# Kernel optimization log

Hardware: AMD Instinct MI355X
Metric: run time of the kernel (lower is better)

Reference implementation:

```python
import jax, jax.numpy as jnp
import numpy as np

B, N, P, D = 16, 358, 72, 96
ND, H, K = 64, 4, 10
HL = H // 2
HG = H - HL
NH = 4  # temporal attention heads


def ln(x, g, b, eps=1e-5):
    m = x.mean(-1, keepdims=True)
    v = ((x - m) ** 2).mean(-1, keepdims=True)
    return (x - m) / jnp.sqrt(v + eps) * g + b


def topk_sparsify(adj, k):
    # row-wise top-k masking + renormalization, vectorized over all leading dims
    shp = adj.shape
    n = shp[-1]
    flat = adj.reshape(-1, shp[-2], n)
    M, R = flat.shape[0], flat.shape[1]
    _, idx = jax.lax.top_k(flat, k)  # (M,R,k)
    mask = jnp.zeros(flat.shape, flat.dtype).at[
        jnp.arange(M)[:, None, None], jnp.arange(R)[None, :, None], idx].set(1.0)
    sp = flat * mask
    sp = sp / (sp.sum(-1, keepdims=True) + 1e-8)
    return sp.reshape(shp)


def forward(patch_features, local_e1, local_e2, global_e1, global_e2, static_e2,
            temperature, pos_enc, wq, bq, wk, bk, wv, bv, wo, bo, tn_g, tn_b,
            de_w1, de_b1, de_g1, de_beta1, de_w2, de_b2, de_g2, de_beta2,
            gnn_w, gnn_b, gnn_g, gnn_beta, gf_w, gf_b,
            ee_w1, ee_b1, ee_g, ee_beta, ee_w2, ee_b2, ee_w3, ee_b3):
    # ---- static multi-head graphs (batched over heads instead of python loop) ----
    adj_l = jax.nn.relu(jnp.einsum('hnd,hdm->hnm', local_e1, local_e2))
    t_l = jnp.clip(temperature[:HL] * 2.0, 0.1, 5.0)
    adj_l = jax.nn.softmax(adj_l / t_l[:, None, None], axis=-1)
    adj_g = jax.nn.relu(jnp.einsum('hnd,hdm->hnm', global_e1, global_e2))
    t_g = jnp.clip(temperature[HL:] * 0.5, 0.1, 2.0)
    adj_g = jax.nn.softmax(adj_g / t_g[:, None, None], axis=-1)
    static_adjs = jnp.concatenate([adj_l, adj_g], axis=0)  # (H,N,N)

    # ---- dynamic graphs ----
    b, n, p, d = patch_features.shape
    pr = patch_features.reshape(b * n, p, d)
    x = pr + pos_enc[:, :p]
    hd = d // NH
    q = (x @ wq + bq).reshape(-1, p, NH, hd).transpose(0, 2, 1, 3)
    kk = (x @ wk + bk).reshape(-1, p, NH, hd).transpose(0, 2, 1, 3)
    v = (x @ wv + bv).reshape(-1, p, NH, hd).transpose(0, 2, 1, 3)
    att = jax.nn.softmax(jnp.einsum('bhqd,bhkd->bhqk', q, kk) / np.float32(np.sqrt(hd)), axis=-1)
    o = jnp.einsum('bhqk,bhkd->bhqd', att, v).transpose(0, 2, 1, 3).reshape(-1, p, d)
    attended = o @ wo + bo  # (BN,P,D)
    imp = jax.nn.softmax(attended.mean(-1), axis=1)  # (BN,P)
    node = (attended * imp[..., None]).sum(1) + pr.mean(1)
    node = ln(node, tn_g, tn_b).reshape(b, n, d)
    h1 = jax.nn.gelu(ln(node @ de_w1 + de_b1, de_g1, de_beta1), approximate=False)
    dyn = ln(h1 @ de_w2 + de_b2, de_g2, de_beta2)  # (B,N,ND)
    for i in range(2):  # 2 structurally distinct GNN layers, batched over B
        sim = jax.nn.softmax(jnp.einsum('bnd,bmd->bnm', dyn, dyn) / 0.2, axis=-1)
        agg = jnp.einsum('bnm,bmd->bnd', sim, dyn)
        out = jax.nn.gelu(ln(agg @ gnn_w[i] + gnn_b[i], gnn_g[i], gnn_beta[i]), approximate=False)
        dyn = out + dyn
    dsim = jax.nn.relu(jnp.einsum('bnd,hdm->bhnm', dyn, static_e2))
    t_d = jnp.clip(temperature, 0.1, 2.0)
    dynamic_adjs = jax.nn.softmax(dsim / t_d[None, :, None, None], axis=-1)  # (B,H,N,N)

    static_adjs = topk_sparsify(static_adjs, K)
    dynamic_adjs = topk_sparsify(dynamic_adjs, K)

    # ---- static/dynamic fusion ----
    node_f = patch_features.mean(2)  # (B,N,D)
    fw = jax.nn.sigmoid(node_f @ gf_w + gf_b)  # (B,N,H)
    w = jnp.transpose(fw, (0, 2, 1))[..., None]  # (B,H,N,1), broadcast over columns
    fused = (1.0 - w) * static_adjs[None] + w * dynamic_adjs  # (B,H,N,N)

    # ---- edge encoder over head dim ----
    mh = jnp.transpose(fused, (0, 2, 3, 1))  # (B,N,N,H)
    e = jax.nn.gelu(ln(mh @ ee_w1 + ee_b1, ee_g, ee_beta), approximate=False)
    e = jax.nn.gelu(e @ ee_w2 + ee_b2, approximate=False)
    e = (e @ ee_w3 + ee_b3)[..., 0]  # (B,N,N)
    final = jax.nn.sigmoid(e) * fused.mean(1)
    return final, static_adjs, dynamic_adjs


def setup_inputs() -> dict:
    key = jax.random.key(0)
    ks = jax.random.split(key, 20)
    r = lambda i, shape, s=0.05: jax.random.normal(ks[i], shape, dtype=jnp.float32) * s
    z = lambda shape: jnp.zeros(shape, jnp.float32)
    o = lambda shape: jnp.ones(shape, jnp.float32)
    return dict(
        patch_features=r(0, (B, N, P, D), 1.0),
        local_e1=r(1, (HL, N, ND // 2), 0.1),
        local_e2=r(2, (HL, ND // 2, N), 0.1),
        global_e1=r(3, (HG, N, ND), 0.1),
        global_e2=r(4, (HG, ND, N), 0.1),
        static_e2=r(5, (H, ND, N), 0.1),
        temperature=jnp.full((H,), 0.5, jnp.float32),
        pos_enc=r(6, (1, 72, D), 0.02),
        wq=r(7, (D, D)), bq=z((D,)),
        wk=r(8, (D, D)), bk=z((D,)),
        wv=r(9, (D, D)), bv=z((D,)),
        wo=r(10, (D, D)), bo=z((D,)),
        tn_g=o((D,)), tn_b=z((D,)),
        de_w1=r(11, (D, 2 * ND)), de_b1=z((2 * ND,)),
        de_g1=o((2 * ND,)), de_beta1=z((2 * ND,)),
        de_w2=r(12, (2 * ND, ND)), de_b2=z((ND,)),
        de_g2=o((ND,)), de_beta2=z((ND,)),
        gnn_w=r(13, (2, ND, ND)), gnn_b=z((2, ND)),
        gnn_g=o((2, ND)), gnn_beta=z((2, ND)),
        gf_w=r(14, (D, H)), gf_b=z((H,)),
        ee_w1=r(15, (H, 4 * H)), ee_b1=z((4 * H,)),
        ee_g=o((4 * H,)), ee_beta=z((4 * H,)),
        ee_w2=r(16, (4 * H, 2 * H)), ee_b2=z((2 * H,)),
        ee_w3=r(17, (2 * H, 1)), ee_b3=z((1,)),
    )


def reference(patch_features, local_e1, local_e2, global_e1, global_e2, static_e2,
              temperature, pos_enc, wq, bq, wk, bk, wv, bv, wo, bo, tn_g, tn_b,
              de_w1, de_b1, de_g1, de_beta1, de_w2, de_b2, de_g2, de_beta2,
              gnn_w, gnn_b, gnn_g, gnn_beta, gf_w, gf_b,
              ee_w1, ee_b1, ee_g, ee_beta, ee_w2, ee_b2, ee_w3, ee_b3):
    return forward(patch_features, local_e1, local_e2, global_e1, global_e2, static_e2,
                   temperature, pos_enc, wq, bq, wk, bk, wv, bv, wo, bo, tn_g, tn_b,
                   de_w1, de_b1, de_g1, de_beta1, de_w2, de_b2, de_g2, de_beta2,
                   gnn_w, gnn_b, gnn_g, gnn_beta, gf_w, gf_b,
                   ee_w1, ee_b1, ee_g, ee_beta, ee_w2, ee_b2, ee_w3, ee_b3)
```

## Files before the change

kernel.cpp:

```cpp
#include <hip/hip_runtime.h>
#include <hip/hip_bf16.h>

#define B_ 16
#define N_ 358
#define P_ 72
#define D_ 96
#define ND_ 64
#define H_ 4
#define NH_ 4
#define HD_ 24
#define K_ 10
#define BN_ (B_*N_)
#define NN_ (N_*N_)
#define RPW_ 6
#define NR5 5

__device__ __forceinline__ float gelu_f(float x){ return 0.5f*x*(1.0f+erff(x*0.7071067811865476f)); }
__device__ __forceinline__ float sigm_f(float x){ return 1.0f/(1.0f+expf(-x)); }

__global__ __launch_bounds__(512, 2) void attn_kernel(
    const float* __restrict__ patch, const float* __restrict__ pos,
    const float* __restrict__ wq, const float* __restrict__ bq,
    const float* __restrict__ wk, const float* __restrict__ bk,
    const float* __restrict__ wv, const float* __restrict__ bv,
    const float* __restrict__ wo, const float* __restrict__ bo,
    const float* __restrict__ tng, const float* __restrict__ tnb,
    float* __restrict__ node_out, float* __restrict__ meanpr_out)
{
    __shared__ __align__(16) float pool[14904];
    __shared__ float rr[80];
    __shared__ float nb[D_];
    __shared__ float st2[2];

    float* const xs   = pool;
    float* const qh   = pool;
    float* const khT  = pool + 2240;
    float* const vhT  = pool + 4568;
    float* const att  = pool + 6584;
    float* const obuf = pool + 12664;
    float* const ats  = pool;

    const int tid = threadIdx.x;
    const int tc  = tid & 31;
    const int tr  = tid >> 5;
    const int rbase = tr * NR5;
    const int bn  = blockIdx.x;
    const float* pr = patch + (size_t)bn * (P_*D_);

    float mpr = 0.f;
    if (tid < D_) {
        #pragma unroll 1
        for (int p = 0; p < P_; ++p) mpr += pr[p*D_+tid];
        mpr *= (1.0f/P_);
        meanpr_out[(size_t)bn*D_ + tid] = mpr;
    }

    #pragma unroll 1
    for (int e = tid; e < 80*100; e += 512) {
        const int row = e / 100, col = e - row*100;
        xs[e] = (row < P_ && col < D_) ? (pr[row*D_+col] + pos[row*D_+col]) : 0.f;
    }
    __syncthreads();

    float aq[3][NR5], ak[3][NR5], av[3][NR5];

#define P1_LOOP(WP, BP, ACC)                                                 \
    {                                                                        \
        _Pragma("unroll")                                                    \
        for (int j = 0; j < 3; ++j) {                                        \
            const float vb = BP[tc + 32*j];                                  \
            _Pragma("unroll")                                                \
            for (int i = 0; i < NR5; ++i) ACC[j][i] = vb;                    \
        }                                                                    \
        _Pragma("unroll 1")                                                  \
        for (int k0 = 0; k0 < D_; k0 += 4) {                                 \
            float4 xv[NR5];                                                  \
            _Pragma("unroll")                                                \
            for (int i = 0; i < NR5; ++i)                                    \
                xv[i] = *reinterpret_cast<const float4*>(&xs[(rbase+i)*100 + k0]); \
            float w4[3][4];                                                  \
            _Pragma("unroll")                                                \
            for (int j = 0; j < 3; ++j) {                                    \
                const int c = tc + 32*j;                                     \
                _Pragma("unroll")                                            \
                for (int kk = 0; kk < 4; ++kk)                               \
                    w4[j][kk] = WP[(k0+kk)*D_ + c];                          \
            }                                                                \
            _Pragma("unroll")                                                \
            for (int j = 0; j < 3; ++j)                                      \
                _Pragma("unroll")                                            \
                for (int i = 0; i < NR5; ++i)                                \
                    ACC[j][i] += xv[i].x*w4[j][0] + xv[i].y*w4[j][1]         \
                               + xv[i].z*w4[j][2] + xv[i].w*w4[j][3];        \
        }                                                                    \
    }

    P1_LOOP(wq, bq, aq)
    P1_LOOP(wk, bk, ak)
    P1_LOOP(wv, bv, av)
#undef P1_LOOP

    __syncthreads();

    const float rs = 0.20412414523193154f;

    float ao[3][NR5];
    #pragma unroll
    for (int j = 0; j < 3; ++j) {
        const float vbo = bo[tc + 32*j];
        #pragma unroll
        for (int i = 0; i < NR5; ++i) ao[j][i] = vbo;
    }

    auto stage = [&](int hh) {
        #pragma unroll
        for (int j = 0; j < 3; ++j) {
            const int c = tc + 32*j;
            const int dl = c - HD_*hh;
            if ((unsigned)dl < (unsigned)HD_) {
                #pragma unroll
                for (int i = 0; i < NR5; ++i) {
                    const int row = rbase + i;
                    qh [row*28 + dl] = aq[j][i] * rs;
                    khT[dl*97 + row] = ak[j][i];
                    vhT[dl*84 + row] = av[j][i];
                }
            }
        }
    };

    stage(0);
    __syncthreads();

    #pragma unroll 1
    for (int h = 0; h < NH_; ++h) {
        float sc[3][NR5];
        #pragma unroll
        for (int j = 0; j < 3; ++j)
            #pragma unroll
            for (int i = 0; i < NR5; ++i) sc[j][i] = 0.f;
        #pragma unroll 1
        for (int d0 = 0; d0 < HD_; d0 += 2) {
            float2 qv[NR5];
            #pragma unroll
            for (int i = 0; i < NR5; ++i)
                qv[i] = *reinterpret_cast<const float2*>(&qh[(rbase+i)*28 + d0]);
            float kv[3][2];
            #pragma unroll
            for (int j = 0; j < 3; ++j) {
                const int jn = tc + 32*j;
                kv[j][0] = khT[(d0+0)*97 + jn];
                kv[j][1] = khT[(d0+1)*97 + jn];
            }
            #pragma unroll
            for (int j = 0; j < 3; ++j)
                #pragma unroll
                for (int i = 0; i < NR5; ++i)
                    sc[j][i] += qv[i].x*kv[j][0] + qv[i].y*kv[j][1];
        }

        #pragma unroll
        for (int i = 0; i < NR5; ++i) {
            float m = fmaxf(sc[0][i], sc[1][i]);
            if (tc < 8) m = fmaxf(m, sc[2][i]);
            #pragma unroll
            for (int s = 1; s < 32; s <<= 1) m = fmaxf(m, __shfl_xor(m, s, 32));
            const float e0 = expf(sc[0][i]-m);
            const float e1 = expf(sc[1][i]-m);
            const float e2 = (tc < 8) ? expf(sc[2][i]-m) : 0.f;
            float sm = e0 + e1 + e2;
            #pragma unroll
            for (int s = 1; s < 32; s <<= 1) sm += __shfl_xor(sm, s, 32);
            const float inv = 1.0f/sm;
            const int row = rbase + i;
            att[row*76 + tc]      = e0*inv;
            att[row*76 + tc + 32] = e1*inv;
            if (tc < 8) att[row*76 + tc + 64] = e2*inv;
        }
        __syncthreads();

        if (tc < HD_) {
            float ov[NR5];
            #pragma unroll
            for (int i = 0; i < NR5; ++i) ov[i] = 0.f;
            #pragma unroll 1
            for (int j0 = 0; j0 < P_; j0 += 4) {
                const float4 vv = *reinterpret_cast<const float4*>(&vhT[tc*84 + j0]);
                #pragma unroll
                for (int i = 0; i < NR5; ++i) {
                    const float4 pa = *reinterpret_cast<const float4*>(&att[(rbase+i)*76 + j0]);
                    ov[i] += pa.x*vv.x + pa.y*vv.y + pa.z*vv.z + pa.w*vv.w;
                }
            }
            #pragma unroll
            for (int i = 0; i < NR5; ++i) obuf[(rbase+i)*28 + tc] = ov[i];
        }
        __syncthreads();

        #pragma unroll 1
        for (int d0 = 0; d0 < HD_; d0 += 2) {
            float2 ov2[NR5];
            #pragma unroll
            for (int i = 0; i < NR5; ++i)
                ov2[i] = *reinterpret_cast<const float2*>(&obuf[(rbase+i)*28 + d0]);
            float w2[3][2];
            #pragma unroll
            for (int j = 0; j < 3; ++j) {
                const int c = tc + 32*j;
                w2[j][0] = wo[(HD_*h + d0 + 0)*D_ + c];
                w2[j][1] = wo[(HD_*h + d0 + 1)*D_ + c];
            }
            #pragma unroll
            for (int j = 0; j < 3; ++j)
                #pragma unroll
                for (int i = 0; i < NR5; ++i)
                    ao[j][i] += ov2[i].x*w2[j][0] + ov2[i].y*w2[j][1];
        }
        if (h < NH_-1) stage(h+1);
        __syncthreads();
    }

    #pragma unroll
    for (int j = 0; j < 3; ++j) {
        const int c = tc + 32*j;
        #pragma unroll
        for (int i = 0; i < NR5; ++i) ats[(rbase+i)*100 + c] = ao[j][i];
    }
    __syncthreads();

    if (tid < P_) {
        const float* ar = ats + tid*100;
        float s = 0.f;
        #pragma unroll 1
        for (int d = 0; d < D_; ++d) s += ar[d];
        rr[tid] = s*(1.0f/D_);
    }
    __syncthreads();
    if (tid < 64) {
        const float a0 = rr[tid];
        const float a1 = (tid < 8) ? rr[64+tid] : -3.0e38f;
        float mx = fmaxf(a0, a1);
        #pragma unroll
        for (int s = 1; s < 64; s <<= 1) mx = fmaxf(mx, __shfl_xor(mx, s));
        const float e0 = expf(a0-mx);
        const float e1 = (tid < 8) ? expf(a1-mx) : 0.f;
        float sm = e0 + e1;
        #pragma unroll
        for (int s = 1; s < 64; s <<= 1) sm += __shfl_xor(sm, s);
        const float inv = 1.0f/sm;
        rr[tid] = e0*inv;
        if (tid < 8) rr[64+tid] = e1*inv;
    }
    __syncthreads();
    if (tid < D_) {
        float s = 0.f;
        #pragma unroll 1
        for (int i = 0; i < P_; ++i) s += ats[i*100+tid]*rr[i];
        nb[tid] = s + mpr;
    }
    __syncthreads();
    if (tid < 64) {
        const float x0 = nb[tid];
        const float x1 = (tid < 32) ? nb[64+tid] : 0.f;
        float sm = x0 + x1;
        float sq = x0*x0 + x1*x1;
        #pragma unroll
        for (int s = 1; s < 64; s <<= 1) { sm += __shfl_xor(sm, s); sq += __shfl_xor(sq, s); }
        if (tid == 0) {
            const float m = sm*(1.0f/D_);
            const float v = sq*(1.0f/D_) - m*m;
            st2[0] = m; st2[1] = rsqrtf(v + 1e-5f);
        }
    }
    __syncthreads();
    if (tid < D_) {
        const float y = (nb[tid]-st2[0])*st2[1]*tng[tid] + tnb[tid];
        node_out[(size_t)bn*D_+tid] = y;
    }
}

__global__ __launch_bounds__(128) void enc1_kernel(
    const float* __restrict__ node, const float* __restrict__ w1, const float* __restrict__ b1,
    const float* __restrict__ g1, const float* __restrict__ be1, float* __restrict__ h1)
{
    __shared__ float nr[D_];
    __shared__ float buf[128];
    __shared__ float st2[2];
    const int tid = threadIdx.x; const int bn = blockIdx.x;
    if (tid < D_) nr[tid] = node[(size_t)bn*D_+tid];
    __syncthreads();
    float s = b1[tid];
    for (int c = 0; c < D_; ++c) s += nr[c]*w1[c*128+tid];
    buf[tid] = s;
    __syncthreads();
    if (tid == 0) {
        float m=0.f; for(int d=0;d<128;++d) m+=buf[d]; m *= (1.0f/128.0f);
        float v=0.f; for(int d=0;d<128;++d){ float df=buf[d]-m; v+=df*df; } v *= (1.0f/128.0f);
        st2[0]=m; st2[1]=rsqrtf(v+1e-5f);
    }
    __syncthreads();
    float y = (buf[tid]-st2[0])*st2[1]*g1[tid] + be1[tid];
    h1[(size_t)bn*128+tid] = gelu_f(y);
}

__global__ __launch_bounds__(64) void enc2_kernel(
    const float* __restrict__ h1, const float* __restrict__ w2, const float* __restrict__ b2,
    const float* __restrict__ g2, const float* __restrict__ be2, float* __restrict__ dyn)
{
    __shared__ float hr[128];
    __shared__ float buf[ND_];
    __shared__ float st2[2];
    const int tid = threadIdx.x; const int bn = blockIdx.x;
    hr[tid] = h1[(size_t)bn*128+tid];
    hr[tid+64] = h1[(size_t)bn*128+64+tid];
    __syncthreads();
    float s = b2[tid];
    for (int c = 0; c < 128; ++c) s += hr[c]*w2[c*ND_+tid];
    buf[tid] = s;
    __syncthreads();
    if (tid == 0) {
        float m=0.f; for(int d=0;d<ND_;++d) m+=buf[d]; m *= (1.0f/ND_);
        float v=0.f; for(int d=0;d<ND_;++d){ float df=buf[d]-m; v+=df*df; } v *= (1.0f/ND_);
        st2[0]=m; st2[1]=rsqrtf(v+1e-5f);
    }
    __syncthreads();
    dyn[(size_t)bn*ND_+tid] = (buf[tid]-st2[0])*st2[1]*g2[tid] + be2[tid];
}

__global__ __launch_bounds__(256) void gnn_kernel(
    const float* __restrict__ din, float* __restrict__ dout,
    const float* __restrict__ gw, const float* __restrict__ gb,
    const float* __restrict__ gg, const float* __restrict__ gbe, int layer)
{
    __shared__ float dq[ND_];
    __shared__ float prob[N_];
    __shared__ float red[256];
    __shared__ float aggp[4*ND_];
    __shared__ float buf[ND_];
    __shared__ float st2[2];
    const int tid = threadIdx.x; const int bn = blockIdx.x;
    const int b = bn / N_;
    const float* base = din + (size_t)b*N_*ND_;
    if (tid < ND_) dq[tid] = din[(size_t)bn*ND_+tid];
    __syncthreads();

    float lmax = -1e30f;
    for (int m = tid; m < N_; m += 256) {
        const float* rm = base + (size_t)m*ND_;
        float s = 0.f;
        for (int c = 0; c < ND_; ++c) s += dq[c]*rm[c];
        s *= 5.0f;
        prob[m] = s;
        lmax = fmaxf(lmax, s);
    }
    red[tid]=lmax; __syncthreads();
    for (int st=128; st>0; st>>=1){ if(tid<st) red[tid]=fmaxf(red[tid],red[tid+st]); __syncthreads(); }
    const float mx = red[0]; __syncthreads();
    float lsum = 0.f;
    for (int m=tid; m<N_; m+=256){ float ev=expf(prob[m]-mx); prob[m]=ev; lsum+=ev; }
    red[tid]=lsum; __syncthreads();
    for (int st=128; st>0; st>>=1){ if(tid<st) red[tid]+=red[tid+st]; __syncthreads(); }
    const float inv = 1.0f/red[0]; __syncthreads();
    for (int m=tid; m<N_; m+=256) prob[m]*=inv;
    __syncthreads();

    {
        const int part = tid >> 6, d = tid & 63;
        float s = 0.f;
        for (int m = part; m < N_; m += 4) s += prob[m]*base[(size_t)m*ND_+d];
        aggp[part*ND_+d] = s;
    }
    __syncthreads();
    if (tid < ND_)
        aggp[tid] = aggp[tid]+aggp[ND_+tid]+aggp[2*ND_+tid]+aggp[3*ND_+tid];
    __syncthreads();
    if (tid < ND_) {
        float t = gb[layer*ND_+tid];
        for (int c = 0; c < ND_; ++c) t += aggp[c]*gw[(layer*ND_+c)*ND_+tid];
        buf[tid] = t;
    }
    __syncthreads();
    if (tid == 0) {
        float m=0.f; for(int d=0;d<ND_;++d) m+=buf[d]; m *= (1.0f/ND_);
        float v=0.f; for(int d=0;d<ND_;++d){ float df=buf[d]-m; v+=df*df; } v *= (1.0f/ND_);
        st2[0]=m; st2[1]=rsqrtf(v+1e-5f);
    }
    __syncthreads();
    if (tid < ND_) {
        float y = (buf[tid]-st2[0])*st2[1]*gg[layer*ND_+tid] + gbe[layer*ND_+tid];
        dout[(size_t)bn*ND_+tid] = gelu_f(y) + dq[tid];
    }
}

__device__ __forceinline__ void wave_softmax_topk_store(
    float lv[RPW_], int lane, float* __restrict__ outrow)
{
    float mx = 0.f;
    #pragma unroll
    for (int j=0;j<RPW_;++j) mx = fmaxf(mx, lv[j]);
    #pragma unroll
    for (int s=1;s<64;s<<=1) mx = fmaxf(mx, __shfl_xor(mx, s));
    float sm = 0.f;
    #pragma unroll
    for (int j=0;j<RPW_;++j) {
        const int m = lane + 64*j;
        const float e = (m < N_) ? expf(lv[j]-mx) : 0.f;
        lv[j] = e; sm += e;
    }
    #pragma unroll
    for (int s=1;s<64;s<<=1) sm += __shfl_xor(sm, s);
    const float inv = 1.0f/sm;
    #pragma unroll
    for (int j=0;j<RPW_;++j) lv[j] *= inv;

    unsigned sel = 0u;
    float ksum = 0.f;
    for (int it = 0; it < K_; ++it) {
        float bv = -1.f; int bm = 0x7fffffff;
        #pragma unroll
        for (int j=0;j<RPW_;++j) {
            const int m = lane + 64*j;
            if (m < N_ && !((sel>>j)&1u) && lv[j] > bv) { bv = lv[j]; bm = m; }
        }
        #pragma unroll
        for (int s=1;s<64;s<<=1) {
            const float ov = __shfl_xor(bv, s);
            const int   om = __shfl_xor(bm, s);
            if (ov > bv || (ov == bv && om < bm)) { bv = ov; bm = om; }
        }
        ksum += bv;
        if ((bm & 63) == lane) sel |= 1u << (bm >> 6);
    }
    const float dn = 1.0f/(ksum + 1e-8f);
    #pragma unroll
    for (int j=0;j<RPW_;++j) {
        const int m = lane + 64*j;
        if (m < N_) outrow[m] = ((sel>>j)&1u) ? lv[j]*dn : 0.f;
    }
}

__global__ __launch_bounds__(256) void static_adj_kernel(
    const float* __restrict__ le1, const float* __restrict__ le2,
    const float* __restrict__ ge1, const float* __restrict__ ge2,
    const float* __restrict__ temp, float* __restrict__ outs)
{
    __shared__ float e1l[4][ND_];
    const int tid = threadIdx.x;
    const int wv = tid >> 6, lane = tid & 63;
    const int r = blockIdx.x*4 + wv;
    const int h = r / N_, n = r % N_;
    if (h < 2) { if (lane < 32) e1l[wv][lane] = le1[(h*N_+n)*32+lane]; }
    else       { e1l[wv][lane] = ge1[((h-2)*N_+n)*64+lane]; }
    __syncthreads();
    const float t = temp[h];
    const float tl = (h < 2) ? fminf(fmaxf(t*2.0f,0.1f),5.0f) : fminf(fmaxf(t*0.5f,0.1f),2.0f);
    const float invt = 1.0f/tl;
    float lv[RPW_];
    #pragma unroll
    for (int j=0;j<RPW_;++j) lv[j] = 0.f;
    if (h < 2) {
        for (int c = 0; c < 32; ++c) {
            const float dc = e1l[wv][c];
            const float* sr = le2 + (size_t)(h*32+c)*N_;
            #pragma unroll
            for (int j=0;j<RPW_;++j) {
                const int m = lane + 64*j;
                if (m < N_) lv[j] += dc*sr[m];
            }
        }
    } else {
        for (int c = 0; c < 64; ++c) {
            const float dc = e1l[wv][c];
            const float* sr = ge2 + (size_t)((h-2)*64+c)*N_;
            #pragma unroll
            for (int j=0;j<RPW_;++j) {
                const int m = lane + 64*j;
                if (m < N_) lv[j] += dc*sr[m];
            }
        }
    }
    #pragma unroll
    for (int j=0;j<RPW_;++j) lv[j] = fmaxf(lv[j],0.f)*invt;
    wave_softmax_topk_store(lv, lane, outs + (size_t)r*N_);
}

__global__ __launch_bounds__(256) void dyn_adj_kernel(
    const float* __restrict__ dyn, const float* __restrict__ se2,
    const float* __restrict__ temp, float* __restrict__ outd)
{
    __shared__ float dql[4][ND_];
    const int tid = threadIdx.x;
    const int wv = tid >> 6, lane = tid & 63;
    const int r = blockIdx.x*4 + wv;
    const int b = r / (H_*N_);
    const int rem = r % (H_*N_);
    const int h = rem / N_, n = rem % N_;
    dql[wv][lane] = dyn[((size_t)(b*N_+n))*ND_ + lane];
    __syncthreads();
    const float invt = 1.0f/fminf(fmaxf(temp[h],0.1f),2.0f);
    float lv[RPW_];
    #pragma unroll
    for (int j=0;j<RPW_;++j) lv[j] = 0.f;
    const float* sb = se2 + (size_t)h*ND_*N_;
    for (int c = 0; c < ND_; ++c) {
        const float dc = dql[wv][c];
        const float* sr = sb + (size_t)c*N_;
        #pragma unroll
        for (int j=0;j<RPW_;++j) {
            const int m = lane + 64*j;
            if (m < N_) lv[j] += dc*sr[m];
        }
    }
    #pragma unroll
    for (int j=0;j<RPW_;++j) lv[j] = fmaxf(lv[j],0.f)*invt;
    wave_softmax_topk_store(lv, lane, outd + ((size_t)(b*H_+h)*N_+n)*(size_t)N_);
}

__global__ __launch_bounds__(256) void fw_kernel(
    const float* __restrict__ meanpr, const float* __restrict__ gfw,
    const float* __restrict__ gfb, float* __restrict__ wf)
{
    const int gid = blockIdx.x*256 + threadIdx.x;
    if (gid >= BN_*H_) return;
    const int bn = gid >> 2, h = gid & 3;
    float s = gfb[h];
    const float* mp = meanpr + (size_t)bn*D_;
    for (int c=0;c<D_;++c) s += mp[c]*gfw[c*H_+h];
    wf[gid] = sigm_f(s);
}

__global__ __launch_bounds__(256) void edge_kernel(
    const float* __restrict__ staticf, const float* __restrict__ dynf,
    const float* __restrict__ wf,
    const float* __restrict__ ew1, const float* __restrict__ eb1,
    const float* __restrict__ eg,  const float* __restrict__ ebe,
    const float* __restrict__ ew2, const float* __restrict__ eb2,
    const float* __restrict__ ew3, const float* __restrict__ eb3,
    float* __restrict__ outf)
{
    __shared__ float w1s[64], w2s[128], b1s[16], gs[16], bes[16], b2s[8], w3s[8];
    __shared__ float b3v;
    const int tid = threadIdx.x;
    if (tid < 64)                 w1s[tid]     = ew1[tid];
    else if (tid < 192)           w2s[tid-64]  = ew2[tid-64];
    else if (tid < 208)           b1s[tid-192] = eb1[tid-192];
    else if (tid < 224)           gs[tid-208]  = eg[tid-208];
    else if (tid < 240)           bes[tid-224] = ebe[tid-224];
    else if (tid < 248)           b2s[tid-240] = eb2[tid-240];
    else                          w3s[tid-248] = ew3[tid-248];
    if (tid == 0) b3v = eb3[0];
    __syncthreads();

    const size_t gid = (size_t)blockIdx.x*256 + tid;
    if (gid >= (size_t)B_*NN_) return;
    const int m = (int)(gid % N_);
    const size_t t1 = gid / N_;
    const int n = (int)(t1 % N_);
    const int b = (int)(t1 / N_);

    const float* wrow = wf + ((size_t)(b*N_+n))*4;
    float mh[4]; float msum = 0.f;
    #pragma unroll
    for (int h=0; h<4; ++h) {
        float w  = wrow[h];
        float st = staticf[((size_t)(h*N_+n))*N_ + m];
        float da = dynf[(((size_t)(b*4+h))*N_+n)*(size_t)N_ + m];
        float f = (1.0f-w)*st + w*da;
        mh[h] = f; msum += f;
    }
    float e16[16]; float mean = 0.f;
    #pragma unroll
    for (int j=0;j<16;++j) {
        float s = b1s[j];
        #pragma unroll
        for (int h=0;h<4;++h) s += mh[h]*w1s[h*16+j];
        e16[j] = s; mean += s;
    }
    mean *= (1.0f/16.0f);
    float var = 0.f;
    #pragma unroll
    for (int j=0;j<16;++j){ float df=e16[j]-mean; var += df*df; }
    var *= (1.0f/16.0f);
    const float rinv = rsqrtf(var + 1e-5f);
    #pragma unroll
    for (int j=0;j<16;++j) e16[j] = gelu_f((e16[j]-mean)*rinv*gs[j] + bes[j]);
    float e8[8];
    #pragma unroll
    for (int o=0;o<8;++o) {
        float s = b2s[o];
        #pragma unroll
        for (int j=0;j<16;++j) s += e16[j]*w2s[j*8+o];
        e8[o] = gelu_f(s);
    }
    float e = b3v;
    #pragma unroll
    for (int o=0;o<8;++o) e += e8[o]*w3s[o];
    outf[gid] = sigm_f(e) * (msum*0.25f);
}

extern "C" void kernel_launch(void* const* d_in, const int* in_sizes, int n_in,
                              void* d_out, int out_size, void* d_ws, size_t ws_size,
                              hipStream_t stream)
{
    const float* patch = (const float*)d_in[0];
    const float* le1   = (const float*)d_in[1];
    const float* le2   = (const float*)d_in[2];
    const float* ge1   = (const float*)d_in[3];
    const float* ge2   = (const float*)d_in[4];
    const float* se2   = (const float*)d_in[5];
    const float* temp  = (const float*)d_in[6];
    const float* pos   = (const float*)d_in[7];
    const float* wq    = (const float*)d_in[8];
    const float* bq    = (const float*)d_in[9];
    const float* wk    = (const float*)d_in[10];
    const float* bk    = (const float*)d_in[11];
    const float* wv    = (const float*)d_in[12];
    const float* bv    = (const float*)d_in[13];
    const float* wo    = (const float*)d_in[14];
    const float* bo    = (const float*)d_in[15];
    const float* tng   = (const float*)d_in[16];
    const float* tnb   = (const float*)d_in[17];
    const float* dw1   = (const float*)d_in[18];
    const float* db1   = (const float*)d_in[19];
    const float* dg1   = (const float*)d_in[20];
    const float* dbe1  = (const float*)d_in[21];
    const float* dw2   = (const float*)d_in[22];
    const float* db2   = (const float*)d_in[23];
    const float* dg2   = (const float*)d_in[24];
    const float* dbe2  = (const float*)d_in[25];
    const float* gw    = (const float*)d_in[26];
    const float* gb    = (const float*)d_in[27];
    const float* gg    = (const float*)d_in[28];
    const float* gbe   = (const float*)d_in[29];
    const float* gfw   = (const float*)d_in[30];
    const float* gfb   = (const float*)d_in[31];
    const float* ew1   = (const float*)d_in[32];
    const float* eb1   = (const float*)d_in[33];
    const float* eg    = (const float*)d_in[34];
    const float* ebe   = (const float*)d_in[35];
    const float* ew2   = (const float*)d_in[36];
    const float* eb2   = (const float*)d_in[37];
    const float* ew3   = (const float*)d_in[38];
    const float* eb3   = (const float*)d_in[39];
    (void)in_sizes; (void)n_in; (void)out_size; (void)ws_size;

    float* ws      = (float*)d_ws;
    float* meanpr  = ws;
    float* node    = meanpr + (size_t)BN_*D_;
    float* h1      = node   + (size_t)BN_*D_;
    float* dyn0    = h1     + (size_t)BN_*128;
    float* dyn1    = node;
    float* wfuse   = h1;

    float* out        = (float*)d_out;
    float* out_final  = out;
    float* out_static = out + (size_t)B_*NN_;
    float* out_dyn    = out_static + (size_t)H_*NN_;

    attn_kernel<<<BN_, 512, 0, stream>>>(patch,pos,wq,bq,wk,bk,wv,bv,wo,bo,tng,tnb,node,meanpr);
    enc1_kernel<<<BN_, 128, 0, stream>>>(node,dw1,db1,dg1,dbe1,h1);
    enc2_kernel<<<BN_, 64,  0, stream>>>(h1,dw2,db2,dg2,dbe2,dyn0);
    gnn_kernel<<<BN_, 256, 0, stream>>>(dyn0,dyn1,gw,gb,gg,gbe,0);
    gnn_kernel<<<BN_, 256, 0, stream>>>(dyn1,dyn0,gw,gb,gg,gbe,1);
    static_adj_kernel<<<H_*N_/4, 256, 0, stream>>>(le1,le2,ge1,ge2,temp,out_static);
    dyn_adj_kernel<<<B_*H_*N_/4, 256, 0, stream>>>(dyn0,se2,temp,out_dyn);
    fw_kernel<<<(BN_*H_+255)/256, 256, 0, stream>>>(meanpr,gfw,gfb,wfuse);
    edge_kernel<<<((size_t)B_*NN_+255)/256, 256, 0, stream>>>(
        out_static,out_dyn,wfuse,ew1,eb1,eg,ebe,ew2,eb2,ew3,eb3,out_final);
}
```

Measured before the change: 2.969 ms.

## Pre-transpose attention weights and vectorize QKV, score and output projections

Adds a small kernel that transposes wq/wk/wv/wo into workspace so the attention kernel can read weights as float4 along the reduction dimension instead of scalar strided loads. K is now stored row-major with a 28-float stride, so score dot products read float4 from both Q and K. Softmax exponentials switch to fast __expf. This trades an extra launch, more shared memory and possible LDS bank conflicts for fewer load instructions, with slightly lower exp precision.

```diff
diff --git a/kernel.cpp b/kernel.cpp
--- a/kernel.cpp
+++ b/kernel.cpp
@@ -18,26 +18,42 @@
 __device__ __forceinline__ float gelu_f(float x){ return 0.5f*x*(1.0f+erff(x*0.7071067811865476f)); }
 __device__ __forceinline__ float sigm_f(float x){ return 1.0f/(1.0f+expf(-x)); }
 
+__global__ __launch_bounds__(256) void transw_kernel(
+    const float* __restrict__ wq, const float* __restrict__ wk,
+    const float* __restrict__ wv, const float* __restrict__ wo,
+    float* __restrict__ wqT, float* __restrict__ wkT,
+    float* __restrict__ wvT, float* __restrict__ woT)
+{
+    const int gid = blockIdx.x*256 + threadIdx.x;
+    if (gid >= 4*D_*D_) return;
+    const int mat = gid / (D_*D_);
+    const int idx = gid - mat*(D_*D_);
+    const int c = idx / D_, k = idx - c*D_;
+    const float* src = (mat==0)?wq:(mat==1)?wk:(mat==2)?wv:wo;
+    float* dst = (mat==0)?wqT:(mat==1)?wkT:(mat==2)?wvT:woT;
+    dst[idx] = src[k*D_ + c];
+}
+
 __global__ __launch_bounds__(512, 2) void attn_kernel(
     const float* __restrict__ patch, const float* __restrict__ pos,
-    const float* __restrict__ wq, const float* __restrict__ bq,
-    const float* __restrict__ wk, const float* __restrict__ bk,
-    const float* __restrict__ wv, const float* __restrict__ bv,
-    const float* __restrict__ wo, const float* __restrict__ bo,
+    const float* __restrict__ wqT, const float* __restrict__ bq,
+    const float* __restrict__ wkT, const float* __restrict__ bk,
+    const float* __restrict__ wvT, const float* __restrict__ bv,
+    const float* __restrict__ woT, const float* __restrict__ bo,
     const float* __restrict__ tng, const float* __restrict__ tnb,
     float* __restrict__ node_out, float* __restrict__ meanpr_out)
 {
-    __shared__ __align__(16) float pool[14904];
+    __shared__ __align__(16) float pool[15264];
     __shared__ float rr[80];
     __shared__ float nb[D_];
     __shared__ float st2[2];
 
     float* const xs   = pool;
     float* const qh   = pool;
-    float* const khT  = pool + 2240;
-    float* const vhT  = pool + 4568;
-    float* const att  = pool + 6584;
-    float* const obuf = pool + 12664;
+    float* const kh   = pool + 2240;
+    float* const vhT  = pool + 4928;
+    float* const att  = pool + 6944;
+    float* const obuf = pool + 13024;
     float* const ats  = pool;
 
     const int tid = threadIdx.x;
@@ -64,7 +80,7 @@
 
     float aq[3][NR5], ak[3][NR5], av[3][NR5];
 
-#define P1_LOOP(WP, BP, ACC)                                                 \
+#define P1_LOOP(WTP, BP, ACC)                                                \
     {                                                                        \
         _Pragma("unroll")                                                    \
         for (int j = 0; j < 3; ++j) {                                        \
@@ -78,26 +94,22 @@
             _Pragma("unroll")                                                \
             for (int i = 0; i < NR5; ++i)                                    \
                 xv[i] = *reinterpret_cast<const float4*>(&xs[(rbase+i)*100 + k0]); \
-            float w4[3][4];                                                  \
+            float4 w4[3];                                                    \
             _Pragma("unroll")                                                \
-            for (int j = 0; j < 3; ++j) {                                    \
-                const int c = tc + 32*j;                                     \
-                _Pragma("unroll")                                            \
-                for (int kk = 0; kk < 4; ++kk)                               \
-                    w4[j][kk] = WP[(k0+kk)*D_ + c];                          \
-            }                                                                \
+            for (int j = 0; j < 3; ++j)                                      \
+                w4[j] = *reinterpret_cast<const float4*>(&WTP[(tc+32*j)*D_ + k0]); \
             _Pragma("unroll")                                                \
             for (int j = 0; j < 3; ++j)                                      \
                 _Pragma("unroll")                                            \
                 for (int i = 0; i < NR5; ++i)                                \
-                    ACC[j][i] += xv[i].x*w4[j][0] + xv[i].y*w4[j][1]         \
-                               + xv[i].z*w4[j][2] + xv[i].w*w4[j][3];        \
+                    ACC[j][i] += xv[i].x*w4[j].x + xv[i].y*w4[j].y           \
+                               + xv[i].z*w4[j].z + xv[i].w*w4[j].w;          \
         }                                                                    \
     }
 
-    P1_LOOP(wq, bq, aq)
-    P1_LOOP(wk, bk, ak)
-    P1_LOOP(wv, bv, av)
+    P1_LOOP(wqT, bq, aq)
+    P1_LOOP(wkT, bk, ak)
+    P1_LOOP(wvT, bv, av)
 #undef P1_LOOP
 
     __syncthreads();
@@ -122,7 +134,7 @@
                 for (int i = 0; i < NR5; ++i) {
                     const int row = rbase + i;
                     qh [row*28 + dl] = aq[j][i] * rs;
-                    khT[dl*97 + row] = ak[j][i];
+                    kh [row*28 + dl] = ak[j][i];
                     vhT[dl*84 + row] = av[j][i];
                 }
             }
@@ -140,23 +152,23 @@
             #pragma unroll
             for (int i = 0; i < NR5; ++i) sc[j][i] = 0.f;
         #pragma unroll 1
-        for (int d0 = 0; d0 < HD_; d0 += 2) {
-            float2 qv[NR5];
+        for (int d0 = 0; d0 < HD_; d0 += 4) {
+            float4 qv[NR5];
             #pragma unroll
             for (int i = 0; i < NR5; ++i)
-                qv[i] = *reinterpret_cast<const float2*>(&qh[(rbase+i)*28 + d0]);
-            float kv[3][2];
+                qv[i] = *reinterpret_cast<const float4*>(&qh[(rbase+i)*28 + d0]);
+            float4 kv[3];
             #pragma unroll
             for (int j = 0; j < 3; ++j) {
                 const int jn = tc + 32*j;
-                kv[j][0] = khT[(d0+0)*97 + jn];
-                kv[j][1] = khT[(d0+1)*97 + jn];
+                kv[j] = *reinterpret_cast<const float4*>(&kh[jn*28 + d0]);
             }
             #pragma unroll
             for (int j = 0; j < 3; ++j)
                 #pragma unroll
                 for (int i = 0; i < NR5; ++i)
-                    sc[j][i] += qv[i].x*kv[j][0] + qv[i].y*kv[j][1];
+                    sc[j][i] += qv[i].x*kv[j].x + qv[i].y*kv[j].y
+                              + qv[i].z*kv[j].z + qv[i].w*kv[j].w;
         }
 
         #pragma unroll
@@ -165,9 +177,9 @@
             if (tc < 8) m = fmaxf(m, sc[2][i]);
             #pragma unroll
             for (int s = 1; s < 32; s <<= 1) m = fmaxf(m, __shfl_xor(m, s, 32));
-            const float e0 = expf(sc[0][i]-m);
-            const float e1 = expf(sc[1][i]-m);
-            const float e2 = (tc < 8) ? expf(sc[2][i]-m) : 0.f;
+            const float e0 = __expf(sc[0][i]-m);
+            const float e1 = __expf(sc[1][i]-m);
+            const float e2 = (tc < 8) ? __expf(sc[2][i]-m) : 0.f;
             float sm = e0 + e1 + e2;
             #pragma unroll
             for (int s = 1; s < 32; s <<= 1) sm += __shfl_xor(sm, s, 32);
@@ -198,23 +210,21 @@
         __syncthreads();
 
         #pragma unroll 1
-        for (int d0 = 0; d0 < HD_; d0 += 2) {
-            float2 ov2[NR5];
+        for (int d0 = 0; d0 < HD_; d0 += 4) {
+            float4 ov4[NR5];
             #pragma unroll
             for (int i = 0; i < NR5; ++i)
-                ov2[i] = *reinterpret_cast<const float2*>(&obuf[(rbase+i)*28 + d0]);
-            float w2[3][2];
-            #pragma unroll
-            for (int j = 0; j < 3; ++j) {
-                const int c = tc + 32*j;
-                w2[j][0] = wo[(HD_*h + d0 + 0)*D_ + c];
-                w2[j][1] = wo[(HD_*h + d0 + 1)*D_ + c];
-            }
+                ov4[i] = *reinterpret_cast<const float4*>(&obuf[(rbase+i)*28 + d0]);
+            float4 w4[3];
+            #pragma unroll
+            for (int j = 0; j < 3; ++j)
+                w4[j] = *reinterpret_cast<const float4*>(&woT[(tc+32*j)*D_ + HD_*h + d0]);
             #pragma unroll
             for (int j = 0; j < 3; ++j)
                 #pragma unroll
                 for (int i = 0; i < NR5; ++i)
-                    ao[j][i] += ov2[i].x*w2[j][0] + ov2[i].y*w2[j][1];
+                    ao[j][i] += ov4[i].x*w4[j].x + ov4[i].y*w4[j].y
+                              + ov4[i].z*w4[j].z + ov4[i].w*w4[j].w;
         }
         if (h < NH_-1) stage(h+1);
         __syncthreads();
@@ -242,8 +252,8 @@
         float mx = fmaxf(a0, a1);
         #pragma unroll
         for (int s = 1; s < 64; s <<= 1) mx = fmaxf(mx, __shfl_xor(mx, s));
-        const float e0 = expf(a0-mx);
-        const float e1 = (tid < 8) ? expf(a1-mx) : 0.f;
+        const float e0 = __expf(a0-mx);
+        const float e1 = (tid < 8) ? __expf(a1-mx) : 0.f;
         float sm = e0 + e1;
         #pragma unroll
         for (int s = 1; s < 64; s <<= 1) sm += __shfl_xor(sm, s);
@@ -651,13 +661,18 @@
     float* dyn0    = h1     + (size_t)BN_*128;
     float* dyn1    = node;
     float* wfuse   = h1;
+    float* wqT     = dyn0   + (size_t)BN_*ND_;
+    float* wkT     = wqT + D_*D_;
+    float* wvT     = wkT + D_*D_;
+    float* woT     = wvT + D_*D_;
 
     float* out        = (float*)d_out;
     float* out_final  = out;
     float* out_static = out + (size_t)B_*NN_;
     float* out_dyn    = out_static + (size_t)H_*NN_;
 
-    attn_kernel<<<BN_, 512, 0, stream>>>(patch,pos,wq,bq,wk,bk,wv,bv,wo,bo,tng,tnb,node,meanpr);
+    transw_kernel<<<(4*D_*D_+255)/256, 256, 0, stream>>>(wq,wk,wv,wo,wqT,wkT,wvT,woT);
+    attn_kernel<<<BN_, 512, 0, stream>>>(patch,pos,wqT,bq,wkT,bk,wvT,bv,woT,bo,tng,tnb,node,meanpr);
     enc1_kernel<<<BN_, 128, 0, stream>>>(node,dw1,db1,dg1,dbe1,h1);
     enc2_kernel<<<BN_, 64,  0, stream>>>(h1,dw2,db2,dg2,dbe2,dyn0);
     gnn_kernel<<<BN_, 256, 0, stream>>>(dyn0,dyn1,gw,gb,gg,gbe,0);
```

Result: slower. 3.519 ms (+18.5%).
